# Kernel tuning notes

Measured on AMD Instinct MI355X. Metric: run time of the kernel, lower is better.

Reference implementation:

```python
import jax, jax.numpy as jnp
import numpy as np

K = 20          # neighbors per point
EPS = 1e-5      # BatchNorm eps
SLOPE = 0.2     # LeakyReLU negative slope


def _knn(x, k):
    # x: [B, C, N] -> idx [B, N, k] of nearest neighbors in feature space
    sq = jnp.sum(x * x, axis=1)                       # [B, N]
    inner = jnp.einsum('bcn,bcm->bnm', x, x)          # [B, N, N]
    neg_dist = 2.0 * inner - sq[:, :, None] - sq[:, None, :]
    _, idx = jax.lax.top_k(neg_dist, k)
    return idx


def _edge_features(x, idx):
    # x: [B, C, N], idx: [B, N, k] -> edge features [B, 2C, N, k] = cat(x_i, x_j - x_i)
    xt = jnp.transpose(x, (0, 2, 1))                  # [B, N, C]
    nb = jax.vmap(lambda f, i: f[i])(xt, idx)         # [B, N, k, C]
    center = jnp.broadcast_to(xt[:, :, None, :], nb.shape)
    ef = jnp.concatenate([center, nb - center], axis=-1)  # [B, N, k, 2C]
    return jnp.transpose(ef, (0, 3, 1, 2))            # [B, 2C, N, k]


def _bn(t, g, b, axes):
    # BatchNorm (training-mode batch stats), channel axis = 1
    m = jnp.mean(t, axis=axes, keepdims=True)
    v = jnp.var(t, axis=axes, keepdims=True)
    tn = (t - m) * jax.lax.rsqrt(v + EPS)
    shp = [1] * t.ndim
    shp[1] = -1
    return tn * g.reshape(shp) + b.reshape(shp)


def _lrelu(t):
    return jnp.where(t >= 0, t, SLOPE * t)


def _layer2d(t, w, g, b):
    # 1x1 Conv2d (no bias) + BN2d + LeakyReLU over edge tensor [B, C, N, k]
    t = jnp.einsum('bcnk,oc->bonk', t, w)
    return _lrelu(_bn(t, g, b, (0, 2, 3)))


def _multi_edge_conv(x, w1, g1, b1, w2, g2, b2):
    idx = _knn(x, K)
    t = _edge_features(x, idx)
    t = _layer2d(t, w1, g1, b1)
    t = _layer2d(t, w2, g2, b2)
    return jnp.max(t, axis=-1)                        # max over neighbors -> [B, O, N]


def _edge_conv(x, w, g, b):
    idx = _knn(x, K)
    t = _edge_features(x, idx)
    t = _layer2d(t, w, g, b)
    return jnp.max(t, axis=-1)


def _tail(x, w, g, b):
    # 1x1 Conv1d (no bias) + BN1d + LeakyReLU, x: [B, 256, N] -> [B, 128, N]
    t = jnp.einsum('bcn,oc->bon', x, w)
    return _lrelu(_bn(t, g, b, (0, 2)))


def setup_inputs() -> dict:
    key = jax.random.key(0)
    ks = jax.random.split(key, 16)
    B, C, N = 8, 6, 2048

    def w(k, o, i):
        return jax.random.normal(k, (o, i), jnp.float32) * np.sqrt(2.0 / i).astype(np.float32)

    d = {
        'x': jax.random.normal(ks[0], (B, C, N), jnp.float32),
        # MultiEdgeConvolution 0: edge dim 2*6=12 -> 64 -> 64
        'w0a': w(ks[1], 64, 12), 'g0a': jnp.ones(64), 'b0a': jnp.zeros(64),
        'w0b': w(ks[2], 64, 64), 'g0b': jnp.ones(64), 'b0b': jnp.zeros(64),
        # MultiEdgeConvolution 1: edge dim 2*64=128 -> 64 -> 64
        'w1a': w(ks[3], 64, 128), 'g1a': jnp.ones(64), 'b1a': jnp.zeros(64),
        'w1b': w(ks[4], 64, 64), 'g1b': jnp.ones(64), 'b1b': jnp.zeros(64),
        # EdgeConvolution 2 and 3: 128 -> 64
        'w2': w(ks[5], 64, 128), 'g2': jnp.ones(64), 'b2': jnp.zeros(64),
        'w3': w(ks[6], 64, 128), 'g3': jnp.ones(64), 'b3': jnp.zeros(64),
        # Tail: 256 -> 128
        'wt': w(ks[7], 128, 256), 'gt': jnp.ones(128), 'bt': jnp.zeros(128),
    }
    return d


def reference(x, w0a, g0a, b0a, w0b, g0b, b0b,
              w1a, g1a, b1a, w1b, g1b, b1b,
              w2, g2, b2, w3, g3, b3, wt, gt, bt):
    x1 = _multi_edge_conv(x,  w0a, g0a, b0a, w0b, g0b, b0b)   # [B, 64, N]
    x2 = _multi_edge_conv(x1, w1a, g1a, b1a, w1b, g1b, b1b)   # [B, 64, N]
    x3 = _edge_conv(x2, w2, g2, b2)                           # [B, 64, N]
    x4 = _edge_conv(x3, w3, g3, b3)                           # [B, 64, N]
    feats = jnp.concatenate([x1, x2, x3, x4], axis=1)         # [B, 256, N]
    return _tail(feats, wt, gt, bt)                           # [B, 128, N]
```

## Files before the change

### kernel.cpp

```cpp
#include <hip/hip_runtime.h>

constexpr int BB = 8, NN = 2048, KK = 20;
constexpr float SLP = 0.2f;
constexpr float NEG = -3.0e38f;
constexpr float EMPTYV = -3.3e38f;
constexpr double EPSD = 1e-5;

typedef short short8 __attribute__((ext_vector_type(8)));
typedef float f32x4 __attribute__((ext_vector_type(4)));
typedef unsigned short ushort;

__device__ __forceinline__ float lrelu(float v) { return v >= 0.f ? v : SLP * v; }

__device__ __forceinline__ float bits2f(unsigned u) { union { unsigned u; float f; } a; a.u = u; return a.f; }
__device__ __forceinline__ unsigned f2bits(float f) { union { float f; unsigned u; } a; a.f = f; return a.u; }

__device__ __forceinline__ ushort bf16rne(float f) {
  unsigned u = f2bits(f);
  return (ushort)((u + 0x7fffu + ((u >> 16) & 1u)) >> 16);
}

__device__ __forceinline__ void split3(float x, ushort& h, ushort& m, ushort& l) {
  h = bf16rne(x);
  float fh = bits2f(((unsigned)h) << 16);
  float t1 = x - fh;
  m = bf16rne(t1);
  float fm = bits2f(((unsigned)m) << 16);
  float t2 = t1 - fm;
  l = bf16rne(t2);
}

__global__ __launch_bounds__(256) void k_prep0(const float* __restrict__ x, float* __restrict__ x0nc,
                                               ushort* __restrict__ xh, ushort* __restrict__ xm,
                                               ushort* __restrict__ xlo, float* __restrict__ sqb) {
  int i = blockIdx.x * 256 + threadIdx.x;
  if (i >= BB * NN) return;
  int b = i >> 11, n = i & (NN - 1);
  float v[6];
#pragma unroll
  for (int c = 0; c < 6; ++c) v[c] = x[((size_t)b * 6 + c) * NN + n];
  float s = 0.f;
#pragma unroll
  for (int c = 0; c < 6; ++c) s = __fadd_rn(s, __fmul_rn(v[c], v[c]));
  sqb[i] = s;
#pragma unroll
  for (int c = 0; c < 6; ++c) x0nc[(size_t)i * 6 + c] = v[c];
  size_t base = (size_t)i * 32;
#pragma unroll
  for (int c = 0; c < 32; ++c) {
    float xv = (c < 6) ? v[c] : 0.f;
    ushort h, m, l;
    split3(xv, h, m, l);
    xh[base + c] = h; xm[base + c] = m; xlo[base + c] = l;
  }
}

__global__ __launch_bounds__(256) void k_prepC(const float* __restrict__ xs, ushort* __restrict__ xh,
                                               ushort* __restrict__ xm, ushort* __restrict__ xlo,
                                               float* __restrict__ sqb) {
  int i = blockIdx.x * 256 + threadIdx.x;
  if (i >= BB * NN) return;
  const float* src = xs + (size_t)i * 64;
  float v[64];
#pragma unroll
  for (int c4 = 0; c4 < 16; ++c4) {
    float4 t = *reinterpret_cast<const float4*>(src + 4 * c4);
    v[4 * c4 + 0] = t.x; v[4 * c4 + 1] = t.y; v[4 * c4 + 2] = t.z; v[4 * c4 + 3] = t.w;
  }
  float s = 0.f;
#pragma unroll
  for (int c = 0; c < 64; ++c) s = __fadd_rn(s, __fmul_rn(v[c], v[c]));
  sqb[i] = s;
  size_t base = (size_t)i * 64;
#pragma unroll
  for (int c = 0; c < 64; ++c) {
    ushort h, m, l;
    split3(v[c], h, m, l);
    xh[base + c] = h; xm[base + c] = m; xlo[base + c] = l;
  }
}

template <int CP>
__global__ __launch_bounds__(256) void k_gram(const ushort* __restrict__ xh, const ushort* __restrict__ xm,
                                              const ushort* __restrict__ xlo, const float* __restrict__ sqb,
                                              float* __restrict__ S, int b0) {
  constexpr int KS = CP / 32;
  const int bl = blockIdx.z, b = b0 + bl;
  const int r0 = blockIdx.x * 32;
  const int cc0 = blockIdx.y * 32;
  const int tid = threadIdx.x, w = tid >> 6, l = tid & 63;
  const int rt = w & 1;
  const size_t xb = (size_t)b * NN * CP;
  const int ko = (l >> 4) * 8;

  short8 Ah[KS], Am[KS], Al[KS];
  const int ar = r0 + rt * 16 + (l & 15);
#pragma unroll
  for (int ks = 0; ks < KS; ++ks) {
    size_t o = xb + (size_t)ar * CP + ks * 32 + ko;
    Ah[ks] = *reinterpret_cast<const short8*>(xh + o);
    Am[ks] = *reinterpret_cast<const short8*>(xm + o);
    Al[ks] = *reinterpret_cast<const short8*>(xlo + o);
  }
  float sqi[4];
  const int rr = r0 + rt * 16 + (l >> 4) * 4;
#pragma unroll
  for (int q = 0; q < 4; ++q) sqi[q] = sqb[b * NN + rr + q];
  const size_t Sbase = ((size_t)bl * NN + rr) * NN;

  int ct = cc0 + (w >> 1);
  short8 Bh[KS], Bm[KS], Bl[KS], Ch[KS], Cm[KS], Cl[KS];
#pragma unroll
  for (int ks = 0; ks < KS; ++ks) {
    size_t o = xb + (size_t)(ct * 16 + (l & 15)) * CP + ks * 32 + ko;
    Bh[ks] = *reinterpret_cast<const short8*>(xh + o);
    Bm[ks] = *reinterpret_cast<const short8*>(xm + o);
    Bl[ks] = *reinterpret_cast<const short8*>(xlo + o);
  }
  for (int t = 0; t < 16; ++t) {
    int nct = ct + 2;
    if (t < 15) {
#pragma unroll
      for (int ks = 0; ks < KS; ++ks) {
        size_t o = xb + (size_t)(nct * 16 + (l & 15)) * CP + ks * 32 + ko;
        Ch[ks] = *reinterpret_cast<const short8*>(xh + o);
        Cm[ks] = *reinterpret_cast<const short8*>(xm + o);
        Cl[ks] = *reinterpret_cast<const short8*>(xlo + o);
      }
    }
    f32x4 acc = {0.f, 0.f, 0.f, 0.f};
#pragma unroll
    for (int ks = 0; ks < KS; ++ks) {
      acc = __builtin_amdgcn_mfma_f32_16x16x32_bf16(Am[ks], Bm[ks], acc, 0, 0, 0);
      acc = __builtin_amdgcn_mfma_f32_16x16x32_bf16(Ah[ks], Bl[ks], acc, 0, 0, 0);
      acc = __builtin_amdgcn_mfma_f32_16x16x32_bf16(Al[ks], Bh[ks], acc, 0, 0, 0);
      acc = __builtin_amdgcn_mfma_f32_16x16x32_bf16(Ah[ks], Bm[ks], acc, 0, 0, 0);
      acc = __builtin_amdgcn_mfma_f32_16x16x32_bf16(Am[ks], Bh[ks], acc, 0, 0, 0);
      acc = __builtin_amdgcn_mfma_f32_16x16x32_bf16(Ah[ks], Bh[ks], acc, 0, 0, 0);
    }
    int col = ct * 16 + (l & 15);
    float sqj = sqb[b * NN + col];
#pragma unroll
    for (int q = 0; q < 4; ++q) {
      float sc = __fsub_rn(__fsub_rn(2.f * acc[q], sqi[q]), sqj);
      S[Sbase + (size_t)q * NN + col] = sc;
    }
#pragma unroll
    for (int ks = 0; ks < KS; ++ks) { Bh[ks] = Ch[ks]; Bm[ks] = Cm[ks]; Bl[ks] = Cl[ks]; }
    ct = nct;
  }
}

__global__ __launch_bounds__(256) void k_select(const float* __restrict__ S, int* __restrict__ idxo, int b0) {
  const int bl = blockIdx.y, b = b0 + bl;
  const int wv = threadIdx.x >> 6, l = threadIdx.x & 63;
  const int row = blockIdx.x * 4 + wv;
  __shared__ float sr[4][2048];
  __shared__ int oid[4][20];
  char* base = reinterpret_cast<char*>(&sr[wv][0]);
  const float* Sp = S + ((size_t)bl * NN + row) * NN;
#pragma unroll
  for (int e = 0; e < 8; ++e) {
    float4 v = *reinterpret_cast<const float4*>(Sp + e * 256 + l * 4);
    int c = e * 64 + l;
    c ^= (c >> 3) & 7;
    *reinterpret_cast<float4*>(base + (c << 4)) = v;
  }
  float v0 = EMPTYV, v1 = EMPTYV;
  int i0 = -1, i1 = -1;
#pragma unroll
  for (int e = 0; e < 8; ++e) {
    int c = l * 8 + e;
    c ^= (c >> 3) & 7;
    float4 v = *reinterpret_cast<const float4*>(base + (c << 4));
    int jb = l * 32 + e * 4;
    float va[4] = {v.x, v.y, v.z, v.w};
#pragma unroll
    for (int q = 0; q < 4; ++q) {
      float vv = va[q];
      int jj = jb + q;
      if (vv > v0) { v1 = v0; i1 = i0; v0 = vv; i0 = jj; }
      else if (vv > v1) { v1 = vv; i1 = jj; }
    }
  }
  for (int e = 0; e < KK; ++e) {
    float m = v0;
#pragma unroll
    for (int d = 1; d < 64; d <<= 1) m = fmaxf(m, __shfl_xor(m, d));
    unsigned long long msk = __ballot(v0 == m);
    int wl = __ffsll((unsigned long long)msk) - 1;
    if (l == wl) {
      oid[wv][e] = i0;
      int j = i0;
      int cc = j >> 2;
      int cs = cc ^ ((cc >> 3) & 7);
      *reinterpret_cast<float*>(base + (cs << 4) + ((j & 3) << 2)) = NEG;
      v0 = v1; i0 = i1; v1 = EMPTYV; i1 = -1;
      if (v0 <= EMPTYV) {
        v0 = EMPTYV; v1 = EMPTYV; i0 = -1; i1 = -1;
#pragma unroll
        for (int e2 = 0; e2 < 8; ++e2) {
          int c = l * 8 + e2;
          c ^= (c >> 3) & 7;
          float4 v = *reinterpret_cast<const float4*>(base + (c << 4));
          int jb = l * 32 + e2 * 4;
          float va[4] = {v.x, v.y, v.z, v.w};
#pragma unroll
          for (int q = 0; q < 4; ++q) {
            float vv = va[q];
            int jj = jb + q;
            if (vv > v0) { v1 = v0; i1 = i0; v0 = vv; i0 = jj; }
            else if (vv > v1) { v1 = vv; i1 = jj; }
          }
        }
      }
    }
  }
  if (l < KK) idxo[((size_t)b * NN + row) * KK + l] = oid[wv][l];
}

template <int C>
__global__ __launch_bounds__(256) void k_uv(const float* __restrict__ xin, const float* __restrict__ w,
                                            float* __restrict__ u, float* __restrict__ v) {
  const int b = blockIdx.y, n0 = blockIdx.x * 4;
  const int tid = threadIdx.x, o = tid & 63, nn = tid >> 6;
  __shared__ float wl[64][2 * C + 1];
  __shared__ float xl[4][C];
  for (int t = tid; t < 64 * 2 * C; t += 256) wl[t / (2 * C)][t % (2 * C)] = w[t];
  for (int t = tid; t < 4 * C; t += 256) xl[t / C][t % C] = xin[((size_t)b * NN + n0 + t / C) * C + t % C];
  __syncthreads();
  float s1 = 0.f, s2 = 0.f;
#pragma unroll
  for (int c = 0; c < C; ++c) {
    float xv = xl[nn][c];
    s1 = fmaf(wl[o][c], xv, s1);
    s2 = fmaf(wl[o][C + c], xv, s2);
  }
  size_t i = ((size_t)b * NN + n0 + nn) * 64 + o;
  u[i] = s1 - s2;
  v[i] = s2;
}

__global__ __launch_bounds__(256) void k_passA(const float* __restrict__ u, const float* __restrict__ v,
                                               const int* __restrict__ idx, double* __restrict__ st) {
  const int b = blockIdx.y, n0 = blockIdx.x * 16;
  const int tid = threadIdx.x, c = tid & 63, nw = tid >> 6;
  double s = 0.0, ss = 0.0;
  for (int nn = nw; nn < 16; nn += 4) {
    size_t nb = (size_t)b * NN + n0 + nn;
    float uu = u[nb * 64 + c];
    const int* ip = idx + nb * KK;
#pragma unroll
    for (int k = 0; k < KK; ++k) {
      float val = uu + v[((size_t)b * NN + ip[k]) * 64 + c];
      double dv = (double)val;
      s += dv; ss = fma(dv, dv, ss);
    }
  }
  __shared__ double red[2][4][64];
  red[0][nw][c] = s; red[1][nw][c] = ss;
  __syncthreads();
  if (tid < 64) {
    double S = red[0][0][tid] + red[0][1][tid] + red[0][2][tid] + red[0][3][tid];
    double SS = red[1][0][tid] + red[1][1][tid] + red[1][2][tid] + red[1][3][tid];
    atomicAdd(&st[tid], S);
    atomicAdd(&st[64 + tid], SS);
  }
}

__global__ __launch_bounds__(256) void k_passAmax(const float* __restrict__ u, const float* __restrict__ v,
                                                  const int* __restrict__ idx, float* __restrict__ xout,
                                                  double* __restrict__ st) {
  const int b = blockIdx.y, n0 = blockIdx.x * 16;
  const int tid = threadIdx.x, c = tid & 63, nw = tid >> 6;
  double s = 0.0, ss = 0.0;
  for (int nn = nw; nn < 16; nn += 4) {
    size_t nb = (size_t)b * NN + n0 + nn;
    float uu = u[nb * 64 + c];
    const int* ip = idx + nb * KK;
    float mx = NEG;
#pragma unroll
    for (int k = 0; k < KK; ++k) {
      float val = uu + v[((size_t)b * NN + ip[k]) * 64 + c];
      mx = fmaxf(mx, val);
      double dv = (double)val;
      s += dv; ss = fma(dv, dv, ss);
    }
    xout[nb * 64 + c] = mx;
  }
  __shared__ double red[2][4][64];
  red[0][nw][c] = s; red[1][nw][c] = ss;
  __syncthreads();
  if (tid < 64) {
    double S = red[0][0][tid] + red[0][1][tid] + red[0][2][tid] + red[0][3][tid];
    double SS = red[1][0][tid] + red[1][1][tid] + red[1][2][tid] + red[1][3][tid];
    atomicAdd(&st[tid], S);
    atomicAdd(&st[64 + tid], SS);
  }
}

__global__ __launch_bounds__(256) void k_passB(const float* __restrict__ u, const float* __restrict__ v,
                                               const int* __restrict__ idx, const double* __restrict__ st1,
                                               const float* __restrict__ g1, const float* __restrict__ b1,
                                               const float* __restrict__ w2, float* __restrict__ xout,
                                               double* __restrict__ st2) {
  const int b = blockIdx.y, n0 = blockIdx.x * 8;
  const int tid = threadIdx.x, lane = tid & 63, wv = tid >> 6;
  __shared__ __align__(16) float act[160][64];
  constexpr double invM = 1.0 / (double)(BB * NN * KK);
  double sm = st1[lane] * invM;
  double ad = (double)g1[lane] / sqrt(st1[64 + lane] * invM - sm * sm + EPSD);
  float a = (float)ad;
  float d = (float)((double)b1[lane] - sm * ad);
  float wr[64];
#pragma unroll
  for (int c4 = 0; c4 < 16; ++c4) {
    float4 t4 = *reinterpret_cast<const float4*>(w2 + (size_t)lane * 64 + 4 * c4);
    wr[4 * c4 + 0] = t4.x; wr[4 * c4 + 1] = t4.y; wr[4 * c4 + 2] = t4.z; wr[4 * c4 + 3] = t4.w;
  }
  for (int p = wv; p < 160; p += 4) {
    int nn = p / 20, k = p - nn * 20;
    size_t nb = (size_t)b * NN + n0 + nn;
    int j = idx[nb * KK + k];
    float val = u[nb * 64 + lane] + v[((size_t)b * NN + j) * 64 + lane];
    act[p][lane] = lrelu(fmaf(a, val, d));
  }
  __syncthreads();
  double s2 = 0.0, ss2 = 0.0;
#pragma unroll
  for (int q = 0; q < 2; ++q) {
    int nl = 2 * wv + q;
    float mx = NEG;
#pragma unroll 4
    for (int k = 0; k < KK; ++k) {
      const float* ap = &act[nl * 20 + k][0];
      float a0 = 0.f, a1 = 0.f, a2 = 0.f, a3 = 0.f;
#pragma unroll
      for (int c4 = 0; c4 < 16; ++c4) {
        float4 v4 = *reinterpret_cast<const float4*>(ap + 4 * c4);
        a0 = fmaf(wr[4 * c4 + 0], v4.x, a0);
        a1 = fmaf(wr[4 * c4 + 1], v4.y, a1);
        a2 = fmaf(wr[4 * c4 + 2], v4.z, a2);
        a3 = fmaf(wr[4 * c4 + 3], v4.w, a3);
      }
      float t2v = (a0 + a1) + (a2 + a3);
      mx = fmaxf(mx, t2v);
      double dv = (double)t2v;
      s2 += dv; ss2 = fma(dv, dv, ss2);
    }
    xout[((size_t)b * NN + n0 + nl) * 64 + lane] = mx;
  }
  __syncthreads();
  double* red = reinterpret_cast<double*>(&act[0][0]);
  red[wv * 64 + lane] = s2;
  red[256 + wv * 64 + lane] = ss2;
  __syncthreads();
  if (tid < 64) {
    double S = red[tid] + red[64 + tid] + red[128 + tid] + red[192 + tid];
    double SS = red[256 + tid] + red[320 + tid] + red[384 + tid] + red[448 + tid];
    atomicAdd(&st2[tid], S);
    atomicAdd(&st2[64 + tid], SS);
  }
}

__global__ __launch_bounds__(256) void k_apply(float* __restrict__ xio, const double* __restrict__ st,
                                               const float* __restrict__ g, const float* __restrict__ bb,
                                               double invM) {
  const int b = blockIdx.y, n0 = blockIdx.x * 4;
  const int tid = threadIdx.x, c = tid & 63, nn = tid >> 6;
  double sm = st[c] * invM;
  double ad = (double)g[c] / sqrt(st[64 + c] * invM - sm * sm + EPSD);
  float a = (float)ad;
  float d = (float)((double)bb[c] - sm * ad);
  size_t i = ((size_t)b * NN + n0 + nn) * 64 + c;
  xio[i] = lrelu(fmaf(a, xio[i], d));
}

__global__ __launch_bounds__(256) void k_wtT(const float* __restrict__ wt, float* __restrict__ wtT) {
  int i = blockIdx.x * 256 + threadIdx.x;
  if (i < 128 * 256) { int o = i >> 8, c = i & 255; wtT[c * 128 + o] = wt[i]; }
}

__global__ __launch_bounds__(256) void k_tail(const float* __restrict__ x1, const float* __restrict__ x2,
                                              const float* __restrict__ x3, const float* __restrict__ x4,
                                              const float* __restrict__ wtT, float* __restrict__ tt) {
  const int b = blockIdx.y, n0 = blockIdx.x * 16;
  const int tid = threadIdx.x, og = tid & 31, nt = tid >> 5;
  __shared__ float xc[256][20];
  const float* xs[4] = {x1, x2, x3, x4};
  for (int t = tid; t < 4096; t += 256) {
    int n = t >> 8, c = t & 255;
    xc[c][n] = xs[c >> 6][((size_t)b * NN + n0 + n) * 64 + (c & 63)];
  }
  __syncthreads();
  float acc[4][2];
#pragma unroll
  for (int r = 0; r < 4; ++r) { acc[r][0] = 0.f; acc[r][1] = 0.f; }
#pragma unroll 4
  for (int c = 0; c < 256; ++c) {
    float4 wv = *reinterpret_cast<const float4*>(&wtT[(size_t)c * 128 + 4 * og]);
    float xc0 = xc[c][2 * nt], xc1 = xc[c][2 * nt + 1];
    acc[0][0] = fmaf(wv.x, xc0, acc[0][0]); acc[0][1] = fmaf(wv.x, xc1, acc[0][1]);
    acc[1][0] = fmaf(wv.y, xc0, acc[1][0]); acc[1][1] = fmaf(wv.y, xc1, acc[1][1]);
    acc[2][0] = fmaf(wv.z, xc0, acc[2][0]); acc[2][1] = fmaf(wv.z, xc1, acc[2][1]);
    acc[3][0] = fmaf(wv.w, xc0, acc[3][0]); acc[3][1] = fmaf(wv.w, xc1, acc[3][1]);
  }
#pragma unroll
  for (int q = 0; q < 2; ++q) {
    float4 o4;
    o4.x = acc[0][q]; o4.y = acc[1][q]; o4.z = acc[2][q]; o4.w = acc[3][q];
    *reinterpret_cast<float4*>(&tt[((size_t)b * NN + n0 + 2 * nt + q) * 128 + 4 * og]) = o4;
  }
}

__global__ __launch_bounds__(256) void k_tailstats(const float* __restrict__ tt, double* __restrict__ st) {
  const int tid = threadIdx.x, c = tid & 127, h = tid >> 7;
  const int r0 = blockIdx.x * 32;
  double s = 0.0, ss = 0.0;
  for (int rr = h; rr < 32; rr += 2) {
    double val = (double)tt[(size_t)(r0 + rr) * 128 + c];
    s += val; ss = fma(val, val, ss);
  }
  __shared__ double red[2][2][128];
  red[0][h][c] = s; red[1][h][c] = ss;
  __syncthreads();
  if (tid < 128) {
    atomicAdd(&st[tid], red[0][0][tid] + red[0][1][tid]);
    atomicAdd(&st[128 + tid], red[1][0][tid] + red[1][1][tid]);
  }
}

__global__ __launch_bounds__(256) void k_tailapply(const float* __restrict__ tt, const double* __restrict__ st,
                                                   const float* __restrict__ g, const float* __restrict__ bb,
                                                   float* __restrict__ out) {
  const int b = blockIdx.y, n0 = blockIdx.x * 64;
  const int tid = threadIdx.x;
  __shared__ float tl[128][65];
  constexpr double invM = 1.0 / (double)(BB * NN);
  {
    const int o = tid & 127, h = tid >> 7;
    double sm = st[o] * invM;
    double ad = (double)g[o] / sqrt(st[128 + o] * invM - sm * sm + EPSD);
    float a = (float)ad;
    float d = (float)((double)bb[o] - sm * ad);
    for (int nn2 = h; nn2 < 64; nn2 += 2) {
      float val = tt[((size_t)b * NN + n0 + nn2) * 128 + o];
      tl[o][nn2] = lrelu(fmaf(a, val, d));
    }
  }
  __syncthreads();
  {
    const int nl = tid & 63, ow = tid >> 6;
    for (int o = ow; o < 128; o += 4)
      out[((size_t)b * 128 + o) * NN + n0 + nl] = tl[o][nl];
  }
}

extern "C" void kernel_launch(void* const* d_in, const int* in_sizes, int n_in,
                              void* d_out, int out_size, void* d_ws, size_t ws_size,
                              hipStream_t stream) {
  const float* x = (const float*)d_in[0];
  const float* w0a = (const float*)d_in[1];
  const float* g0a = (const float*)d_in[2];
  const float* b0a = (const float*)d_in[3];
  const float* w0b = (const float*)d_in[4];
  const float* g0b = (const float*)d_in[5];
  const float* b0b = (const float*)d_in[6];
  const float* w1a = (const float*)d_in[7];
  const float* g1a = (const float*)d_in[8];
  const float* b1a = (const float*)d_in[9];
  const float* w1b = (const float*)d_in[10];
  const float* g1b = (const float*)d_in[11];
  const float* b1b = (const float*)d_in[12];
  const float* w2 = (const float*)d_in[13];
  const float* g2 = (const float*)d_in[14];
  const float* b2 = (const float*)d_in[15];
  const float* w3 = (const float*)d_in[16];
  const float* g3 = (const float*)d_in[17];
  const float* b3 = (const float*)d_in[18];
  const float* wt = (const float*)d_in[19];
  const float* gt = (const float*)d_in[20];
  const float* bt = (const float*)d_in[21];
  float* out = (float*)d_out;

  char* p = (char*)d_ws;
  double* stA = (double*)p; p += 2048;
  double* stB = (double*)p; p += 2048;
  double* stT = (double*)p; p += 2048;
  ushort* xh = (ushort*)p; p += (size_t)BB * NN * 64 * 2;
  ushort* xm = (ushort*)p; p += (size_t)BB * NN * 64 * 2;
  ushort* xlo = (ushort*)p; p += (size_t)BB * NN * 64 * 2;
  float* sqb = (float*)p; p += (size_t)BB * NN * 4;
  float* x0nc = (float*)p; p += (size_t)BB * NN * 6 * 4;
  float* x1 = (float*)p; p += (size_t)BB * NN * 64 * 4;
  float* x2 = (float*)p; p += (size_t)BB * NN * 64 * 4;
  float* x3 = (float*)p; p += (size_t)BB * NN * 64 * 4;
  float* x4 = (float*)p; p += (size_t)BB * NN * 64 * 4;
  float* ub = (float*)p; p += (size_t)BB * NN * 64 * 4;
  float* vb = (float*)p; p += (size_t)BB * NN * 64 * 4;
  float* ttl = (float*)p; p += (size_t)BB * NN * 128 * 4;
  float* wtTb = (float*)p; p += 128 * 256 * 4;
  int* idx = (int*)p; p += (size_t)BB * NN * KK * 4;
  size_t base_bytes = (size_t)(p - (char*)d_ws);
  const size_t SBYTES = (size_t)NN * NN * 4;

  float* S;
  int bc;
  if (ws_size >= base_bytes + SBYTES) {
    S = (float*)(((uintptr_t)p + 255) & ~(uintptr_t)255);
    size_t avail = ws_size - ((char*)S - (char*)d_ws);
    bc = (int)(avail / SBYTES);
    if (bc > BB) bc = BB;
    if (bc < 1) { S = ub; bc = 1; }
  } else {
    S = ub;
    bc = 1;
  }

  constexpr double invMe = 1.0 / (double)(BB * NN * KK);
  dim3 blk(256);

  auto knn = [&](int stage) {
    for (int c = 0; c < BB; c += bc) {
      int nb = BB - c < bc ? BB - c : bc;
      if (stage == 0)
        k_gram<32><<<dim3(NN / 32, 4, nb), blk, 0, stream>>>(xh, xm, xlo, sqb, S, c);
      else
        k_gram<64><<<dim3(NN / 32, 4, nb), blk, 0, stream>>>(xh, xm, xlo, sqb, S, c);
      k_select<<<dim3(NN / 4, nb), blk, 0, stream>>>(S, idx, c);
    }
  };

  k_prep0<<<dim3(BB * NN / 256), blk, 0, stream>>>(x, x0nc, xh, xm, xlo, sqb);
  knn(0);
  k_uv<6><<<dim3(NN / 4, BB), blk, 0, stream>>>(x0nc, w0a, ub, vb);
  hipMemsetAsync(stA, 0, 2048, stream);
  k_passA<<<dim3(NN / 16, BB), blk, 0, stream>>>(ub, vb, idx, stA);
  hipMemsetAsync(stB, 0, 2048, stream);
  k_passB<<<dim3(NN / 8, BB), blk, 0, stream>>>(ub, vb, idx, stA, g0a, b0a, w0b, x1, stB);
  k_apply<<<dim3(NN / 4, BB), blk, 0, stream>>>(x1, stB, g0b, b0b, invMe);

  k_prepC<<<dim3(BB * NN / 256), blk, 0, stream>>>(x1, xh, xm, xlo, sqb);
  knn(1);
  k_uv<64><<<dim3(NN / 4, BB), blk, 0, stream>>>(x1, w1a, ub, vb);
  hipMemsetAsync(stA, 0, 2048, stream);
  k_passA<<<dim3(NN / 16, BB), blk, 0, stream>>>(ub, vb, idx, stA);
  hipMemsetAsync(stB, 0, 2048, stream);
  k_passB<<<dim3(NN / 8, BB), blk, 0, stream>>>(ub, vb, idx, stA, g1a, b1a, w1b, x2, stB);
  k_apply<<<dim3(NN / 4, BB), blk, 0, stream>>>(x2, stB, g1b, b1b, invMe);

  k_prepC<<<dim3(BB * NN / 256), blk, 0, stream>>>(x2, xh, xm, xlo, sqb);
  knn(2);
  k_uv<64><<<dim3(NN / 4, BB), blk, 0, stream>>>(x2, w2, ub, vb);
  hipMemsetAsync(stA, 0, 2048, stream);
  k_passAmax<<<dim3(NN / 16, BB), blk, 0, stream>>>(ub, vb, idx, x3, stA);
  k_apply<<<dim3(NN / 4, BB), blk, 0, stream>>>(x3, stA, g2, b2, invMe);

  k_prepC<<<dim3(BB * NN / 256), blk, 0, stream>>>(x3, xh, xm, xlo, sqb);
  knn(3);
  k_uv<64><<<dim3(NN / 4, BB), blk, 0, stream>>>(x3, w3, ub, vb);
  hipMemsetAsync(stA, 0, 2048, stream);
  k_passAmax<<<dim3(NN / 16, BB), blk, 0, stream>>>(ub, vb, idx, x4, stA);
  k_apply<<<dim3(NN / 4, BB), blk, 0, stream>>>(x4, stA, g3, b3, invMe);

  k_wtT<<<dim3(128), blk, 0, stream>>>(wt, wtTb);
  k_tail<<<dim3(NN / 16, BB), blk, 0, stream>>>(x1, x2, x3, x4, wtTb, ttl);
  hipMemsetAsync(stT, 0, 2048, stream);
  k_tailstats<<<dim3(512), blk, 0, stream>>>(ttl, stT);
  k_tailapply<<<dim3(NN / 64, BB), blk, 0, stream>>>(ttl, stT, gt, bt, out);
}
```

Before: 1.078 ms.

## Fuse BN apply into kNN prep and restructure passB second conv

Result: slower. 1.139 ms (+5.7%).

```diff
diff --git a/kernel.cpp b/kernel.cpp
--- a/kernel.cpp
+++ b/kernel.cpp
@@ -55,22 +55,40 @@
   }
 }
 
-__global__ __launch_bounds__(256) void k_prepC(const float* __restrict__ xs, ushort* __restrict__ xh,
-                                               ushort* __restrict__ xm, ushort* __restrict__ xlo,
-                                               float* __restrict__ sqb) {
-  int i = blockIdx.x * 256 + threadIdx.x;
-  if (i >= BB * NN) return;
-  const float* src = xs + (size_t)i * 64;
+__global__ __launch_bounds__(256) void k_applyprep(float* __restrict__ xio, const double* __restrict__ st,
+                                                   const float* __restrict__ g, const float* __restrict__ bb,
+                                                   ushort* __restrict__ xh, ushort* __restrict__ xm,
+                                                   ushort* __restrict__ xlo, float* __restrict__ sqb) {
+  __shared__ float sa[64], sd[64];
+  const int tid = threadIdx.x;
+  if (tid < 64) {
+    constexpr double invM = 1.0 / (double)(BB * NN * KK);
+    double sm = st[tid] * invM;
+    double ad = (double)g[tid] / sqrt(st[64 + tid] * invM - sm * sm + EPSD);
+    sa[tid] = (float)ad;
+    sd[tid] = (float)((double)bb[tid] - sm * ad);
+  }
+  __syncthreads();
+  int i = blockIdx.x * 256 + tid;
+  float* src = xio + (size_t)i * 64;
   float v[64];
 #pragma unroll
   for (int c4 = 0; c4 < 16; ++c4) {
     float4 t = *reinterpret_cast<const float4*>(src + 4 * c4);
     v[4 * c4 + 0] = t.x; v[4 * c4 + 1] = t.y; v[4 * c4 + 2] = t.z; v[4 * c4 + 3] = t.w;
   }
+#pragma unroll
+  for (int c = 0; c < 64; ++c) v[c] = lrelu(fmaf(sa[c], v[c], sd[c]));
   float s = 0.f;
 #pragma unroll
   for (int c = 0; c < 64; ++c) s = __fadd_rn(s, __fmul_rn(v[c], v[c]));
   sqb[i] = s;
+#pragma unroll
+  for (int c4 = 0; c4 < 16; ++c4) {
+    float4 t;
+    t.x = v[4 * c4 + 0]; t.y = v[4 * c4 + 1]; t.z = v[4 * c4 + 2]; t.w = v[4 * c4 + 3];
+    *reinterpret_cast<float4*>(src + 4 * c4) = t;
+  }
   size_t base = (size_t)i * 64;
 #pragma unroll
   for (int c = 0; c < 64; ++c) {
@@ -306,26 +324,53 @@
                                                double* __restrict__ st2) {
   const int b = blockIdx.y, n0 = blockIdx.x * 8;
   const int tid = threadIdx.x, lane = tid & 63, wv = tid >> 6;
-  __shared__ __align__(16) float act[160][64];
+  __shared__ __align__(16) float buf[160][68];
   constexpr double invM = 1.0 / (double)(BB * NN * KK);
   double sm = st1[lane] * invM;
   double ad = (double)g1[lane] / sqrt(st1[64 + lane] * invM - sm * sm + EPSD);
   float a = (float)ad;
   float d = (float)((double)b1[lane] - sm * ad);
-  float wr[64];
-#pragma unroll
-  for (int c4 = 0; c4 < 16; ++c4) {
-    float4 t4 = *reinterpret_cast<const float4*>(w2 + (size_t)lane * 64 + 4 * c4);
-    wr[4 * c4 + 0] = t4.x; wr[4 * c4 + 1] = t4.y; wr[4 * c4 + 2] = t4.z; wr[4 * c4 + 3] = t4.w;
-  }
+
   for (int p = wv; p < 160; p += 4) {
     int nn = p / 20, k = p - nn * 20;
     size_t nb = (size_t)b * NN + n0 + nn;
     int j = idx[nb * KK + k];
     float val = u[nb * 64 + lane] + v[((size_t)b * NN + j) * 64 + lane];
-    act[p][lane] = lrelu(fmaf(a, val, d));
-  }
-  __syncthreads();
+    buf[p][lane] = lrelu(fmaf(a, val, d));
+  }
+  __syncthreads();
+
+  const int row = wv * 64 + lane;
+  const bool active = row < 160;
+  float ar[64];
+  if (active) {
+#pragma unroll
+    for (int c4 = 0; c4 < 16; ++c4) {
+      float4 t4 = *reinterpret_cast<const float4*>(&buf[row][4 * c4]);
+      ar[4 * c4 + 0] = t4.x; ar[4 * c4 + 1] = t4.y;
+      ar[4 * c4 + 2] = t4.z; ar[4 * c4 + 3] = t4.w;
+    }
+  }
+  __syncthreads();
+
+#pragma unroll 2
+  for (int o = 0; o < 64; ++o) {
+    if (active) {
+      const float* wp = w2 + o * 64;
+      float a0 = 0.f, a1 = 0.f, a2 = 0.f, a3 = 0.f;
+#pragma unroll
+      for (int c4 = 0; c4 < 16; ++c4) {
+        float4 w4 = *reinterpret_cast<const float4*>(wp + 4 * c4);
+        a0 = fmaf(w4.x, ar[4 * c4 + 0], a0);
+        a1 = fmaf(w4.y, ar[4 * c4 + 1], a1);
+        a2 = fmaf(w4.z, ar[4 * c4 + 2], a2);
+        a3 = fmaf(w4.w, ar[4 * c4 + 3], a3);
+      }
+      buf[row][o] = (a0 + a1) + (a2 + a3);
+    }
+  }
+  __syncthreads();
+
   double s2 = 0.0, ss2 = 0.0;
 #pragma unroll
   for (int q = 0; q < 2; ++q) {
@@ -333,17 +378,7 @@
     float mx = NEG;
 #pragma unroll 4
     for (int k = 0; k < KK; ++k) {
-      const float* ap = &act[nl * 20 + k][0];
-      float a0 = 0.f, a1 = 0.f, a2 = 0.f, a3 = 0.f;
-#pragma unroll
-      for (int c4 = 0; c4 < 16; ++c4) {
-        float4 v4 = *reinterpret_cast<const float4*>(ap + 4 * c4);
-        a0 = fmaf(wr[4 * c4 + 0], v4.x, a0);
-        a1 = fmaf(wr[4 * c4 + 1], v4.y, a1);
-        a2 = fmaf(wr[4 * c4 + 2], v4.z, a2);
-        a3 = fmaf(wr[4 * c4 + 3], v4.w, a3);
-      }
-      float t2v = (a0 + a1) + (a2 + a3);
+      float t2v = buf[nl * 20 + k][lane];
       mx = fmaxf(mx, t2v);
       double dv = (double)t2v;
       s2 += dv; ss2 = fma(dv, dv, ss2);
@@ -351,7 +386,7 @@
     xout[((size_t)b * NN + n0 + nl) * 64 + lane] = mx;
   }
   __syncthreads();
-  double* red = reinterpret_cast<double*>(&act[0][0]);
+  double* red = reinterpret_cast<double*>(&buf[0][0]);
   red[wv * 64 + lane] = s2;
   red[256 + wv * 64 + lane] = ss2;
   __syncthreads();
@@ -538,25 +573,22 @@
   k_passA<<<dim3(NN / 16, BB), blk, 0, stream>>>(ub, vb, idx, stA);
   hipMemsetAsync(stB, 0, 2048, stream);
   k_passB<<<dim3(NN / 8, BB), blk, 0, stream>>>(ub, vb, idx, stA, g0a, b0a, w0b, x1, stB);
-  k_apply<<<dim3(NN / 4, BB), blk, 0, stream>>>(x1, stB, g0b, b0b, invMe);
-
-  k_prepC<<<dim3(BB * NN / 256), blk, 0, stream>>>(x1, xh, xm, xlo, sqb);
+  k_applyprep<<<dim3(BB * NN / 256), blk, 0, stream>>>(x1, stB, g0b, b0b, xh, xm, xlo, sqb);
+
   knn(1);
   k_uv<64><<<dim3(NN / 4, BB), blk, 0, stream>>>(x1, w1a, ub, vb);
   hipMemsetAsync(stA, 0, 2048, stream);
   k_passA<<<dim3(NN / 16, BB), blk, 0, stream>>>(ub, vb, idx, stA);
   hipMemsetAsync(stB, 0, 2048, stream);
   k_passB<<<dim3(NN / 8, BB), blk, 0, stream>>>(ub, vb, idx, stA, g1a, b1a, w1b, x2, stB);
-  k_apply<<<dim3(NN / 4, BB), blk, 0, stream>>>(x2, stB, g1b, b1b, invMe);
-
-  k_prepC<<<dim3(BB * NN / 256), blk, 0, stream>>>(x2, xh, xm, xlo, sqb);
+  k_applyprep<<<dim3(BB * NN / 256), blk, 0, stream>>>(x2, stB, g1b, b1b, xh, xm, xlo, sqb);
+
   knn(2);
   k_uv<64><<<dim3(NN / 4, BB), blk, 0, stream>>>(x2, w2, ub, vb);
   hipMemsetAsync(stA, 0, 2048, stream);
   k_passAmax<<<dim3(NN / 16, BB), blk, 0, stream>>>(ub, vb, idx, x3, stA);
-  k_apply<<<dim3(NN / 4, BB), blk, 0, stream>>>(x3, stA, g2, b2, invMe);
-
-  k_prepC<<<dim3(BB * NN / 256), blk, 0, stream>>>(x3, xh, xm, xlo, sqb);
+  k_applyprep<<<dim3(BB * NN / 256), blk, 0, stream>>>(x3, stA, g2, b2, xh, xm, xlo, sqb);
+
   knn(3);
   k_uv<64><<<dim3(NN / 4, BB), blk, 0, stream>>>(x3, w3, ub, vb);
   hipMemsetAsync(stA, 0, 2048, stream);
```
